# Kernel tuning notes

Measured on AMD Instinct MI355X. Metric: run time of the kernel, lower is better.

The kernel has to match this reference:

```python
import jax, jax.numpy as jnp
import numpy as np
import math

H = 2048
NH = 16
NKV = 4
HD = H // NH  # 128
N_REP = NH // NKV
EPS = 1e-6


def rms_norm(x, w, eps=1e-6):
    x32 = x.astype(jnp.float32)
    y = x32 * jax.lax.rsqrt(jnp.mean(x32 * x32, axis=-1, keepdims=True) + eps)
    return (y * w.astype(jnp.float32)).astype(x.dtype)


def mha(normed, key_in, val_in, q_w, k_w, v_w, o_w, bias):
    # normed: [b,s,H]; key_in/val_in: [b,n,H]; bias broadcastable to [b,nh,s,n]
    b, s, _ = normed.shape
    n = key_in.shape[1]
    q = (normed @ q_w).reshape(b, s, NH, HD).transpose(0, 2, 1, 3)      # [b,nh,s,d]
    k = (key_in @ k_w).reshape(b, n, NKV, HD).transpose(0, 2, 1, 3)     # [b,nkv,n,d]
    v = (val_in @ v_w).reshape(b, n, NKV, HD).transpose(0, 2, 1, 3)
    k = jnp.repeat(k, N_REP, axis=1)  # GQA expand -> [b,nh,n,d]
    v = jnp.repeat(v, N_REP, axis=1)
    scores = jnp.einsum('bhsd,bhnd->bhsn', q, k) / math.sqrt(HD) + bias
    probs = jax.nn.softmax(scores.astype(jnp.float32), axis=-1).astype(q.dtype)
    out = jnp.einsum('bhsn,bhnd->bhsd', probs, v)
    out = out.transpose(0, 2, 1, 3).reshape(b, s, NH * HD) @ o_w
    return out, probs


def setup_inputs() -> dict:
    key = jax.random.key(0)
    ks = jax.random.split(key, 20)
    B, S, ND, T = 2, 2048, 64, 2048
    w = lambda k, sh: (jax.random.normal(k, sh, dtype=jnp.float32) * 0.02)
    return {
        'hidden_states': jax.random.normal(ks[0], (B, S, H), dtype=jnp.float32),
        'doc_summary_key': jax.random.normal(ks[1], (B, ND, H), dtype=jnp.float32),
        'doc_summary_value': jax.random.normal(ks[2], (B, ND, H), dtype=jnp.float32),
        'doc_summary_mask': jnp.ones((B, ND), dtype=jnp.float32),
        'token_key': jax.random.normal(ks[3], (B, T, H), dtype=jnp.float32),
        'token_value': jax.random.normal(ks[4], (B, T, H), dtype=jnp.float32),
        'token_mask': jnp.ones((B, T), dtype=jnp.float32),
        'cn_w': jnp.ones((H,), dtype=jnp.float32),
        'cq_w': w(ks[5], (H, NH * HD)),
        'ck_w': w(ks[6], (H, NKV * HD)),
        'cv_w': w(ks[7], (H, NKV * HD)),
        'co_w': w(ks[8], (NH * HD, H)),
        'c_gate': jnp.array([-1.0], dtype=jnp.float32),
        'fn_w': jnp.ones((H,), dtype=jnp.float32),
        'fq_w': w(ks[9], (H, NH * HD)),
        'fk_w': w(ks[10], (H, NKV * HD)),
        'fv_w': w(ks[11], (H, NKV * HD)),
        'fo_w': w(ks[12], (NH * HD, H)),
        'f_gate': jnp.array([-1.0], dtype=jnp.float32),
        'doc_token_map': jax.random.randint(ks[13], (B, T), 0, ND, dtype=jnp.int64)
            if jax.config.jax_enable_x64 else jax.random.randint(ks[13], (B, T), 0, ND).astype(jnp.int32),
    }


def reference(hidden_states, doc_summary_key, doc_summary_value, doc_summary_mask,
              token_key, token_value, token_mask,
              cn_w, cq_w, ck_w, cv_w, co_w, c_gate,
              fn_w, fq_w, fk_w, fv_w, fo_w, f_gate,
              doc_token_map):
    # ---- coarse stage: cross-attention over document summaries ----
    normed = rms_norm(hidden_states, cn_w)
    coarse_bias = ((1.0 - doc_summary_mask) * -1e9)[:, None, None, :]  # [b,1,1,nd]
    attn_out, probs = mha(normed, doc_summary_key, doc_summary_value,
                          cq_w, ck_w, cv_w, co_w, coarse_bias)
    doc_scores = probs.mean(axis=(1, 2))  # [b,nd] avg over heads+query positions
    gate_c = jax.nn.sigmoid(c_gate).astype(attn_out.dtype)
    out = hidden_states + gate_c * attn_out

    # ---- fine stage: cross-attention over token KV with log-doc-score bias ----
    log_ds = jnp.log(doc_scores + EPS)
    doc_bias = jnp.take_along_axis(log_ds, doc_token_map, axis=1)  # [b,T]
    pad_bias = (1.0 - token_mask) * -1e9
    fine_bias = (doc_bias + pad_bias)[:, None, None, :]  # [b,1,1,T]
    normed_f = rms_norm(out, fn_w)
    attn_out_f, _ = mha(normed_f, token_key, token_value,
                        fq_w, fk_w, fv_w, fo_w, fine_bias)
    gate_f = jax.nn.sigmoid(f_gate).astype(attn_out_f.dtype)
    final = out + gate_f * attn_out_f
    return final
```

## Files before the change

kernel.cpp:

```cpp
#include <hip/hip_runtime.h>
#include <hip/hip_bf16.h>

typedef unsigned short u16;
typedef unsigned int u32;
typedef __attribute__((ext_vector_type(8))) short bf16x8;
typedef __attribute__((ext_vector_type(4))) float f32x4;

constexpr int NH = 16;
constexpr int H = 2048;
constexpr float SCALE = 0.08838834764831845f;
constexpr float L2E = 1.4426950408889634f;
constexpr float SCALE2 = SCALE * L2E;
constexpr float THR2 = 8.0f * L2E;

__device__ __forceinline__ u16 f2bf(float f) {
    u32 u = __float_as_uint(f);
    u32 r = u + 0x7fffu + ((u >> 16) & 1u);
    return (u16)(r >> 16);
}
__device__ __forceinline__ u32 pack2(float x, float y) {
    return (u32)f2bf(x) | ((u32)f2bf(y) << 16);
}
__device__ __forceinline__ u32 pack2_cvt(float x, float y) {
    __hip_bfloat162 h = __float22bfloat162_rn(float2{x, y});
    return *reinterpret_cast<u32*>(&h);
}

#define GLD_LDS16(gsrc, ldst)                                                  \
    __builtin_amdgcn_global_load_lds(                                          \
        (const __attribute__((address_space(1))) void*)(gsrc),                 \
        (__attribute__((address_space(3))) void*)(ldst), 16, 0, 0)

__global__ __launch_bounds__(256) void cvt_f32_bf16_2(const float* __restrict__ a,
                                                      u16* __restrict__ oa,
                                                      const float* __restrict__ b,
                                                      u16* __restrict__ ob, int n4) {
    int i = blockIdx.x * 256 + threadIdx.x;
    const float* in;
    u16* out;
    if (i < n4) { in = a; out = oa; }
    else if (i < 2 * n4) { i -= n4; in = b; out = ob; }
    else return;
    float4 v = reinterpret_cast<const float4*>(in)[i];
    uint2 o;
    o.x = pack2(v.x, v.y);
    o.y = pack2(v.z, v.w);
    reinterpret_cast<uint2*>(out)[i] = o;
}

__global__ __launch_bounds__(256) void cvt_f32_bf16(const float* __restrict__ in,
                                                    u16* __restrict__ out, int n4) {
    int i = blockIdx.x * 256 + threadIdx.x;
    if (i >= n4) return;
    float4 v = reinterpret_cast<const float4*>(in)[i];
    uint2 o;
    o.x = pack2(v.x, v.y);
    o.y = pack2(v.z, v.w);
    reinterpret_cast<uint2*>(out)[i] = o;
}

__global__ __launch_bounds__(256)
void transpose_cvt4(const float* __restrict__ i0, const float* __restrict__ i1,
                    const float* __restrict__ i2, const float* __restrict__ i3,
                    u16* __restrict__ o0, u16* __restrict__ o1,
                    u16* __restrict__ o2, u16* __restrict__ o3, int K, int N) {
    const float* in = (blockIdx.z == 0) ? i0 : (blockIdx.z == 1) ? i1
                    : (blockIdx.z == 2) ? i2 : i3;
    u16* out = (blockIdx.z == 0) ? o0 : (blockIdx.z == 1) ? o1
             : (blockIdx.z == 2) ? o2 : o3;
    __shared__ u16 tile[32][33];
    int bn = blockIdx.x * 32, bk = blockIdx.y * 32;
    int tx = threadIdx.x & 31, ty = threadIdx.x >> 5;
#pragma unroll
    for (int r = 0; r < 32; r += 8)
        tile[tx][r + ty] = f2bf(in[(size_t)(bk + r + ty) * N + bn + tx]);
    __syncthreads();
#pragma unroll
    for (int r = 0; r < 32; r += 8)
        out[(size_t)(bn + r + ty) * K + bk + tx] = tile[r + ty][tx];
}

__global__ __launch_bounds__(256) void rmsnorm_kernel(const float* __restrict__ x,
                                                      const float* __restrict__ w,
                                                      u16* __restrict__ y) {
    int r = blockIdx.x;
    const float4* xr = reinterpret_cast<const float4*>(x + (size_t)r * H);
    int t = threadIdx.x;
    float4 v0 = xr[t * 2], v1 = xr[t * 2 + 1];
    float ss = v0.x * v0.x + v0.y * v0.y + v0.z * v0.z + v0.w * v0.w
             + v1.x * v1.x + v1.y * v1.y + v1.z * v1.z + v1.w * v1.w;
#pragma unroll
    for (int d = 1; d < 64; d <<= 1) ss += __shfl_xor(ss, d);
    __shared__ float red[4];
    if ((t & 63) == 0) red[t >> 6] = ss;
    __syncthreads();
    float tot = red[0] + red[1] + red[2] + red[3];
    float rs = rsqrtf(tot * (1.0f / H) + 1e-6f);
    const float4* wr = reinterpret_cast<const float4*>(w);
    float4 w0 = wr[t * 2], w1 = wr[t * 2 + 1];
    uint4 o;
    o.x = pack2(v0.x * rs * w0.x, v0.y * rs * w0.y);
    o.y = pack2(v0.z * rs * w0.z, v0.w * rs * w0.w);
    o.z = pack2(v1.x * rs * w1.x, v1.y * rs * w1.y);
    o.w = pack2(v1.z * rs * w1.z, v1.w * rs * w1.w);
    reinterpret_cast<uint4*>(y + (size_t)r * H)[t] = o;
}

template <int MODE, int BN>
__device__ __forceinline__
void gemm_body(const u16* __restrict__ A, const u16* __restrict__ Bt,
               u16* __restrict__ Cb, float* __restrict__ Cf,
               const float* __restrict__ resid, const float* __restrict__ gate_p,
               int N, int K, int brow, int bcol) {
    constexpr int WN = BN / 32;
    constexpr int BWROWS = BN / 4;
    __shared__ u16 As[2][128 * 64];
    __shared__ u16 Bs[2][BN * 64];
    const int t = threadIdx.x;
    const int lane = t & 63, wid = t >> 6;
    const int wm = wid >> 1, wn = wid & 1;
    const int l15 = lane & 15, hi = lane >> 4;
    const int rsw = l15 & 7;

    f32x4 acc[4][WN] = {};
    const int srow = lane >> 3;
    const int sseg = ((lane & 7) ^ srow) * 8;
    const u16* aBase = A + (size_t)(brow + wid * 32 + srow) * K + sseg;
    const u16* bBase = Bt + (size_t)(bcol + wid * BWROWS + srow) * K + sseg;

#define GSTAGE(KT, BF)                                                          \
    do {                                                                        \
        _Pragma("unroll")                                                       \
        for (int u = 0; u < 4; ++u)                                             \
            GLD_LDS16(aBase + (size_t)(u * 8) * K + (KT),                       \
                      &As[BF][(wid * 32 + u * 8) * 64]);                        \
        _Pragma("unroll")                                                       \
        for (int u = 0; u < BWROWS / 8; ++u)                                    \
            GLD_LDS16(bBase + (size_t)(u * 8) * K + (KT),                       \
                      &Bs[BF][(wid * BWROWS + u * 8) * 64]);                    \
    } while (0)

    GSTAGE(0, 0);
    __syncthreads();
    int buf = 0;
    for (int kt = 0; kt < K; kt += 64) {
        if (kt + 64 < K) GSTAGE(kt + 64, buf ^ 1);
        bf16x8 af[4][2], bfr[WN][2];
#pragma unroll
        for (int i = 0; i < 4; ++i) {
            int row = wm * 64 + i * 16 + l15;
#pragma unroll
            for (int ko = 0; ko < 2; ++ko)
                af[i][ko] = *reinterpret_cast<const bf16x8*>(
                    &As[buf][row * 64 + (((ko * 4 + hi) ^ rsw) * 8)]);
        }
#pragma unroll
        for (int j = 0; j < WN; ++j) {
            int row = wn * (BN / 2) + j * 16 + l15;
#pragma unroll
            for (int ko = 0; ko < 2; ++ko)
                bfr[j][ko] = *reinterpret_cast<const bf16x8*>(
                    &Bs[buf][row * 64 + (((ko * 4 + hi) ^ rsw) * 8)]);
        }
#pragma unroll
        for (int ko = 0; ko < 2; ++ko)
#pragma unroll
            for (int i = 0; i < 4; ++i)
#pragma unroll
                for (int j = 0; j < WN; ++j)
                    acc[i][j] = __builtin_amdgcn_mfma_f32_16x16x32_bf16(
                        af[i][ko], bfr[j][ko], acc[i][j], 0, 0, 0);
        __syncthreads();
        buf ^= 1;
    }
#undef GSTAGE

    float g = 0.f;
    if (MODE == 1) g = 1.0f / (1.0f + expf(-gate_p[0]));
    const int r0 = hi * 4, c0 = l15;
#pragma unroll
    for (int i = 0; i < 4; ++i) {
#pragma unroll
        for (int j = 0; j < WN; ++j) {
            int col = bcol + wn * (BN / 2) + j * 16 + c0;
#pragma unroll
            for (int r = 0; r < 4; ++r) {
                int row = brow + wm * 64 + i * 16 + r0 + r;
                float v = acc[i][j][r];
                if (MODE == 0) Cb[(size_t)row * N + col] = f2bf(v);
                else Cf[(size_t)row * N + col] = resid[(size_t)row * N + col] + g * v;
            }
        }
    }
}

template <int MODE, int BN>
__global__ __launch_bounds__(256)
void gemm_tn(const u16* __restrict__ A, const u16* __restrict__ Bt,
             u16* __restrict__ Cb, float* __restrict__ Cf,
             const float* __restrict__ resid, const float* __restrict__ gate_p,
             int M, int N, int K) {
    int nbx = gridDim.x;
    int nwg = nbx * gridDim.y;
    int lin = blockIdx.y * nbx + blockIdx.x;
    if (!(nwg & 7)) { int q = nwg >> 3; lin = (lin & 7) * q + (lin >> 3); }
    gemm_body<MODE, BN>(A, Bt, Cb, Cf, resid, gate_p, N, K,
                        (lin / nbx) * 128, (lin % nbx) * BN);
}

template <int MODE, int BN>
__global__ __launch_bounds__(256)
void gemm_tn_z2(const u16* __restrict__ A0, const u16* __restrict__ B0, u16* __restrict__ C0,
                const u16* __restrict__ A1, const u16* __restrict__ B1, u16* __restrict__ C1,
                int N, int K) {
    const u16* A = blockIdx.z ? A1 : A0;
    const u16* B = blockIdx.z ? B1 : B0;
    u16* C = blockIdx.z ? C1 : C0;
    gemm_body<MODE, BN>(A, B, C, nullptr, nullptr, nullptr, N, K,
                        blockIdx.y * 128, blockIdx.x * BN);
}

__global__ __launch_bounds__(256)
void coarse_attn(const u16* __restrict__ q, const u16* __restrict__ kc,
                 const u16* __restrict__ vc, const float* __restrict__ mask,
                 float* __restrict__ doc_part, u16* __restrict__ attn_c) {
    constexpr int SC = 2048 / 64;
    int bid = blockIdx.x;
    int b = bid / (NH * SC);
    int rem = bid % (NH * SC);
    int h = rem / SC, sc = rem % SC;
    int kv = h >> 2;
    int t = threadIdx.x, lane = t & 63, wid = t >> 6;
    const int l15 = lane & 15, k0 = (lane >> 4) * 8;

    __shared__ u16 Kt[64 * 136];
    __shared__ u16 Vt[128 * 72];
    __shared__ u16 Pt[4][16 * 72];
    __shared__ float p_acc[64];

    {
        int n = t >> 2, s2 = t & 3;
        const u16* src = kc + (size_t)(b * 64 + n) * 512 + kv * 128;
#pragma unroll
        for (int u = 0; u < 4; ++u) {
            int sg = s2 + u * 4;
            *reinterpret_cast<uint4*>(&Kt[n * 136 + sg * 8]) =
                *reinterpret_cast<const uint4*>(src + sg * 8);
        }
    }
    {
        int n = t & 63, dblk = t >> 6;
        const u16* src = vc + (size_t)(b * 64 + n) * 512 + kv * 128 + dblk * 32;
#pragma unroll
        for (int u = 0; u < 4; ++u) {
            u16 tmp[8];
            *reinterpret_cast<uint4*>(tmp) = *reinterpret_cast<const uint4*>(src + u * 8);
#pragma unroll
            for (int e = 0; e < 8; ++e) Vt[(dblk * 32 + u * 8 + e) * 72 + n] = tmp[e];
        }
    }
    if (t < 64) p_acc[t] = 0.f;
    __syncthreads();

    int qrow = sc * 64 + wid * 16 + l15;
    const u16* qsrc = q + (size_t)(b * 2048 + qrow) * 2048 + h * 128;
    bf16x8 af[4];
#pragma unroll
    for (int kk = 0; kk < 4; ++kk)
        af[kk] = *reinterpret_cast<const bf16x8*>(qsrc + kk * 32 + k0);

    f32x4 sc4[4] = {};
#pragma unroll
    for (int kk = 0; kk < 4; ++kk)
#pragma unroll
        for (int j = 0; j < 4; ++j) {
            bf16x8 bfr = *reinterpret_cast<const bf16x8*>(&Kt[(j * 16 + l15) * 136 + kk * 32 + k0]);
            sc4[j] = __builtin_amdgcn_mfma_f32_16x16x32_bf16(af[kk], bfr, sc4[j], 0, 0, 0);
        }

    float s[4][4];
#pragma unroll
    for (int j = 0; j < 4; ++j) {
        float bia = (1.0f - mask[b * 64 + j * 16 + l15]) * (-1e9f * L2E);
#pragma unroll
        for (int r = 0; r < 4; ++r) s[j][r] = sc4[j][r] * SCALE2 + bia;
    }
    float m4[4], l4[4];
#pragma unroll
    for (int r = 0; r < 4; ++r) {
        float m = fmaxf(fmaxf(s[0][r], s[1][r]), fmaxf(s[2][r], s[3][r]));
#pragma unroll
        for (int d = 1; d < 16; d <<= 1) m = fmaxf(m, __shfl_xor(m, d));
        m4[r] = m;
    }
#pragma unroll
    for (int r = 0; r < 4; ++r) {
        float l = 0.f;
#pragma unroll
        for (int j = 0; j < 4; ++j) { s[j][r] = exp2f(s[j][r] - m4[r]); l += s[j][r]; }
#pragma unroll
        for (int d = 1; d < 16; d <<= 1) l += __shfl_xor(l, d);
        l4[r] = l;
    }
#pragma unroll
    for (int j = 0; j < 4; ++j) {
        float cs = 0.f;
#pragma unroll
        for (int r = 0; r < 4; ++r) {
            float pr = s[j][r] / l4[r];
            Pt[wid][((lane >> 4) * 4 + r) * 72 + j * 16 + l15] = f2bf(pr);
            cs += pr;
        }
        cs += __shfl_xor(cs, 16);
        cs += __shfl_xor(cs, 32);
        if (lane < 16) atomicAdd(&p_acc[j * 16 + lane], cs);
    }
    __syncthreads();

    f32x4 o4[8] = {};
#pragma unroll
    for (int kk2 = 0; kk2 < 2; ++kk2) {
        bf16x8 a2 = *reinterpret_cast<const bf16x8*>(&Pt[wid][l15 * 72 + kk2 * 32 + k0]);
#pragma unroll
        for (int j2 = 0; j2 < 8; ++j2) {
            bf16x8 b2 = *reinterpret_cast<const bf16x8*>(&Vt[(j2 * 16 + l15) * 72 + kk2 * 32 + k0]);
            o4[j2] = __builtin_amdgcn_mfma_f32_16x16x32_bf16(a2, b2, o4[j2], 0, 0, 0);
        }
    }
#pragma unroll
    for (int j2 = 0; j2 < 8; ++j2)
#pragma unroll
        for (int r = 0; r < 4; ++r) {
            int row = sc * 64 + wid * 16 + (lane >> 4) * 4 + r;
            attn_c[(size_t)(b * 2048 + row) * 2048 + h * 128 + j2 * 16 + l15] = f2bf(o4[j2][r]);
        }
    if (t < 64) atomicAdd(&doc_part[(blockIdx.x & 7) * 128 + b * 64 + t], p_acc[t]);
}

__global__ __launch_bounds__(256)
void bias_kernel(const float* __restrict__ doc_part, const int* __restrict__ map,
                 const float* __restrict__ tmask, float* __restrict__ bias) {
    __shared__ float lg[128];
    int t = threadIdx.x;
    if (t < 128) {
        float s = 0.f;
#pragma unroll
        for (int i = 0; i < 8; ++i) s += doc_part[i * 128 + t];
        lg[t] = logf(s / 32768.0f + 1e-6f);
    }
    __syncthreads();
    int i = blockIdx.x * 256 + t;
    if (i >= 2 * 2048) return;
    int b = i >> 11;
    bias[i] = (lg[b * 64 + map[i]] + (1.0f - tmask[i]) * -1e9f) * L2E;
}

__global__ __launch_bounds__(256, 2)
void flash_attn(const u16* __restrict__ q, const u16* __restrict__ kf,
                const u16* __restrict__ vT, const float* __restrict__ bias,
                u16* __restrict__ attn_f) {
    int bid = blockIdx.x;
    int b = bid >> 8;
    int rem = bid & 255;
    int h = rem >> 4, sc = rem & 15;
    int kv = h >> 2;
    int t = threadIdx.x, lane = t & 63, wid = t >> 6;
    const int l15 = lane & 15, hi = lane >> 4;
    const int k0 = hi * 8;
    const int rswp = l15 & 7;

    __shared__ u16 Kt[2][64 * 128];
    __shared__ u16 Vt[2][128 * 64];
    __shared__ u16 Pt[4][32 * 64];

    bf16x8 qf4[2][4];
#pragma unroll
    for (int f = 0; f < 2; ++f) {
        int qrow = sc * 128 + wid * 32 + f * 16 + l15;
        const u16* qsrc = q + (size_t)(b * 2048 + qrow) * 2048 + h * 128;
#pragma unroll
        for (int kk = 0; kk < 4; ++kk)
            qf4[f][kk] = *reinterpret_cast<const bf16x8*>(qsrc + kk * 32 + k0);
    }

    const int krl = lane >> 4, kslot = lane & 15;
    const int vrl = lane >> 3, vslot = lane & 7;
    const u16* kbase = kf + (size_t)(b * 2048) * 512 + kv * 128;
    const u16* vbase = vT + (size_t)(kv * 128) * 4096 + b * 2048;
    const float* bbase = bias + b * 2048;

#define STAGE_K(TT, BF)                                                            \
    do {                                                                           \
        _Pragma("unroll")                                                          \
        for (int u = 0; u < 4; ++u) {                                              \
            int row = wid * 16 + u * 4 + krl;                                      \
            const u16* src = kbase + (size_t)((TT) + row) * 512                    \
                             + ((kslot ^ (row & 7)) * 8);                          \
            GLD_LDS16(src, &Kt[BF][(wid * 16 + u * 4) * 128]);                     \
        }                                                                          \
    } while (0)
#define STAGE_V(TT, BF)                                                            \
    do {                                                                           \
        _Pragma("unroll")                                                          \
        for (int u = 0; u < 4; ++u) {                                              \
            int row = wid * 32 + u * 8 + vrl;                                      \
            const u16* src = vbase + (size_t)row * 4096 + (TT)                     \
                             + ((vslot ^ (row & 7)) * 8);                          \
            GLD_LDS16(src, &Vt[BF][(wid * 32 + u * 8) * 64]);                      \
        }                                                                          \
    } while (0)

    float mstate[2] = {-1e30f, -1e30f}, lstate[2] = {0.f, 0.f};
    f32x4 o4[2][8] = {};

    STAGE_K(0, 0);
    STAGE_V(0, 0);
    __syncthreads();
    int par = 0;

    for (int t0 = 0; t0 < 2048; t0 += 64) {
        int t1 = (t0 + 64) & 2047;
        STAGE_K(t1, par ^ 1);
        STAGE_V(t1, par ^ 1);

        f32x4 st0[4] = {}, st1[4] = {};
        __builtin_amdgcn_s_setprio(1);
#pragma unroll
        for (int kk = 0; kk < 4; ++kk)
#pragma unroll
            for (int kb = 0; kb < 4; ++kb) {
                int row = kb * 16 + l15;
                bf16x8 kfrag = *reinterpret_cast<const bf16x8*>(
                    &Kt[par][row * 128 + (((kk * 4 + hi) ^ (row & 7)) * 8)]);
                st0[kb] = __builtin_amdgcn_mfma_f32_16x16x32_bf16(kfrag, qf4[0][kk], st0[kb], 0, 0, 0);
                st1[kb] = __builtin_amdgcn_mfma_f32_16x16x32_bf16(kfrag, qf4[1][kk], st1[kb], 0, 0, 0);
            }
        __builtin_amdgcn_s_setprio(0);

        float p[2][4][4];
        float pmax[2] = {-1e30f, -1e30f};
#pragma unroll
        for (int kb = 0; kb < 4; ++kb) {
            float4 b4 = *reinterpret_cast<const float4*>(bbase + t0 + kb * 16 + hi * 4);
            float bb[4] = {b4.x, b4.y, b4.z, b4.w};
#pragma unroll
            for (int r = 0; r < 4; ++r) {
                float v0 = st0[kb][r] * SCALE2 + bb[r];
                float v1 = st1[kb][r] * SCALE2 + bb[r];
                p[0][kb][r] = v0;
                p[1][kb][r] = v1;
                pmax[0] = fmaxf(pmax[0], v0);
                pmax[1] = fmaxf(pmax[1], v1);
            }
        }
#pragma unroll
        for (int f = 0; f < 2; ++f) {
            pmax[f] = fmaxf(pmax[f], __shfl_xor(pmax[f], 16));
            pmax[f] = fmaxf(pmax[f], __shfl_xor(pmax[f], 32));
        }

        bool need = (pmax[0] > mstate[0] + THR2) || (pmax[1] > mstate[1] + THR2);
        if (__any(need)) {
#pragma unroll
            for (int f = 0; f < 2; ++f) {
                float mnew = fmaxf(mstate[f], pmax[f]);
                float sco = exp2f(mstate[f] - mnew);
                float sco_out[4];
#pragma unroll
                for (int r = 0; r < 4; ++r) sco_out[r] = __shfl(sco, hi * 4 + r);
#pragma unroll
                for (int j2 = 0; j2 < 8; ++j2)
#pragma unroll
                    for (int r = 0; r < 4; ++r) o4[f][j2][r] *= sco_out[r];
                lstate[f] *= sco;
                mstate[f] = mnew;
            }
        }

#pragma unroll
        for (int f = 0; f < 2; ++f) {
            float lt = 0.f;
#pragma unroll
            for (int kb = 0; kb < 4; ++kb)
#pragma unroll
                for (int r = 0; r < 4; ++r) {
                    p[f][kb][r] = exp2f(p[f][kb][r] - mstate[f]);
                    lt += p[f][kb][r];
                }
            lt += __shfl_xor(lt, 16);
            lt += __shfl_xor(lt, 32);
            lstate[f] += lt;
        }

#pragma unroll
        for (int f = 0; f < 2; ++f)
#pragma unroll
            for (int kb = 0; kb < 4; ++kb) {
                uint2 w;
                w.x = pack2_cvt(p[f][kb][0], p[f][kb][1]);
                w.y = pack2_cvt(p[f][kb][2], p[f][kb][3]);
                int idx = (f * 16 + l15) * 64
                        + (((kb * 2 + (hi >> 1)) ^ rswp) * 8) + (hi & 1) * 4;
                *reinterpret_cast<uint2*>(&Pt[wid][idx]) = w;
            }

        __builtin_amdgcn_s_setprio(1);
#pragma unroll
        for (int kc = 0; kc < 2; ++kc) {
            bf16x8 pa0 = *reinterpret_cast<const bf16x8*>(
                &Pt[wid][l15 * 64 + (((kc * 4 + hi) ^ rswp) * 8)]);
            bf16x8 pa1 = *reinterpret_cast<const bf16x8*>(
                &Pt[wid][(16 + l15) * 64 + (((kc * 4 + hi) ^ rswp) * 8)]);
#pragma unroll
            for (int j2 = 0; j2 < 8; ++j2) {
                int d = j2 * 16 + l15;
                bf16x8 vb = *reinterpret_cast<const bf16x8*>(
                    &Vt[par][d * 64 + (((kc * 4 + hi) ^ (d & 7)) * 8)]);
                o4[0][j2] = __builtin_amdgcn_mfma_f32_16x16x32_bf16(pa0, vb, o4[0][j2], 0, 0, 0);
                o4[1][j2] = __builtin_amdgcn_mfma_f32_16x16x32_bf16(pa1, vb, o4[1][j2], 0, 0, 0);
            }
        }
        __builtin_amdgcn_s_setprio(0);
        __syncthreads();
        par ^= 1;
    }
#undef STAGE_K
#undef STAGE_V

#pragma unroll
    for (int f = 0; f < 2; ++f) {
        float linv[4];
#pragma unroll
        for (int r = 0; r < 4; ++r) linv[r] = 1.0f / __shfl(lstate[f], hi * 4 + r);
#pragma unroll
        for (int j2 = 0; j2 < 8; ++j2)
#pragma unroll
            for (int r = 0; r < 4; ++r) {
                int row = sc * 128 + wid * 32 + f * 16 + hi * 4 + r;
                attn_f[(size_t)(b * 2048 + row) * 2048 + h * 128 + j2 * 16 + l15] =
                    f2bf(o4[f][j2][r] * linv[r]);
            }
    }
}

extern "C" void kernel_launch(void* const* d_in, const int* in_sizes, int n_in,
                              void* d_out, int out_size, void* d_ws, size_t ws_size,
                              hipStream_t stream) {
    const float* hidden = (const float*)d_in[0];
    const float* dsk    = (const float*)d_in[1];
    const float* dsv    = (const float*)d_in[2];
    const float* dsmask = (const float*)d_in[3];
    const float* tk     = (const float*)d_in[4];
    const float* tv     = (const float*)d_in[5];
    const float* tmask  = (const float*)d_in[6];
    const float* cn_w   = (const float*)d_in[7];
    const float* cq_w   = (const float*)d_in[8];
    const float* ck_w   = (const float*)d_in[9];
    const float* cv_w   = (const float*)d_in[10];
    const float* co_w   = (const float*)d_in[11];
    const float* c_gate = (const float*)d_in[12];
    const float* fn_w   = (const float*)d_in[13];
    const float* fq_w   = (const float*)d_in[14];
    const float* fk_w   = (const float*)d_in[15];
    const float* fv_w   = (const float*)d_in[16];
    const float* fo_w   = (const float*)d_in[17];
    const float* f_gate = (const float*)d_in[18];
    const int*   map    = (const int*)d_in[19];
    float* out_f = (float*)d_out;

    char* ws = (char*)d_ws;
    size_t off = 0;
    auto alloc = [&](size_t bytes) {
        char* p = ws + off;
        off += (bytes + 255) & ~(size_t)255;
        return p;
    };
    u16*  normA = (u16*)alloc(4096ULL * 2048 * 2);
    u16*  qbuf  = (u16*)alloc(4096ULL * 2048 * 2);
    u16*  kc    = (u16*)alloc(128ULL * 512 * 2);
    u16*  vc    = (u16*)alloc(128ULL * 512 * 2);
    u16*  dskb  = (u16*)alloc(128ULL * 2048 * 2);
    u16*  dsvb  = (u16*)alloc(128ULL * 2048 * 2);
    u16*  kfb   = (u16*)alloc(4096ULL * 512 * 2);
    u16*  vTb   = (u16*)alloc(512ULL * 4096 * 2);
    u16*  cqT   = (u16*)alloc(2048ULL * 2048 * 2);
    u16*  ckT   = (u16*)alloc(512ULL * 2048 * 2);
    u16*  cvT   = (u16*)alloc(512ULL * 2048 * 2);
    u16*  coT   = (u16*)alloc(2048ULL * 2048 * 2);
    u16*  fqT   = (u16*)alloc(2048ULL * 2048 * 2);
    u16*  fkT   = (u16*)alloc(512ULL * 2048 * 2);
    u16*  fvT   = (u16*)alloc(512ULL * 2048 * 2);
    u16*  foT   = (u16*)alloc(2048ULL * 2048 * 2);
    float* doc_part = (float*)alloc(8 * 128 * 4);
    float* biasb    = (float*)alloc(4096 * 4);

    hipMemsetAsync(doc_part, 0, 8 * 128 * 4, stream);

    transpose_cvt4<<<dim3(64, 64, 4), 256, 0, stream>>>(cq_w, co_w, fq_w, fo_w,
                                                        cqT, coT, fqT, foT, 2048, 2048);
    transpose_cvt4<<<dim3(16, 64, 4), 256, 0, stream>>>(ck_w, cv_w, fk_w, fv_w,
                                                        ckT, cvT, fkT, fvT, 2048, 512);

    cvt_f32_bf16_2<<<(2 * 128 * 2048 / 4 + 255) / 256, 256, 0, stream>>>(
        dsk, dskb, dsv, dsvb, 128 * 2048 / 4);
    rmsnorm_kernel<<<4096, 256, 0, stream>>>(hidden, cn_w, normA);

    gemm_tn<0, 128><<<dim3(16, 32), 256, 0, stream>>>(normA, cqT, qbuf, nullptr, nullptr, nullptr, 4096, 2048, 2048);
    gemm_tn_z2<0, 64><<<dim3(8, 1, 2), 256, 0, stream>>>(dskb, ckT, kc, dsvb, cvT, vc, 512, 2048);

    coarse_attn<<<1024, 256, 0, stream>>>(qbuf, kc, vc, dsmask, doc_part, normA);
    bias_kernel<<<16, 256, 0, stream>>>(doc_part, map, tmask, biasb);

    gemm_tn<1, 128><<<dim3(16, 32), 256, 0, stream>>>(normA, coT, nullptr, out_f, hidden, c_gate, 4096, 2048, 2048);

    rmsnorm_kernel<<<4096, 256, 0, stream>>>(out_f, fn_w, qbuf);
    gemm_tn<0, 128><<<dim3(16, 32), 256, 0, stream>>>(qbuf, fqT, normA, nullptr, nullptr, nullptr, 4096, 2048, 2048);
    cvt_f32_bf16<<<(4096 * 2048 / 4 + 255) / 256, 256, 0, stream>>>(tk, qbuf, 4096 * 2048 / 4);
    gemm_tn<0, 64><<<dim3(8, 32), 256, 0, stream>>>(qbuf, fkT, kfb, nullptr, nullptr, nullptr, 4096, 512, 2048);
    cvt_f32_bf16<<<(4096 * 2048 / 4 + 255) / 256, 256, 0, stream>>>(tv, qbuf, 4096 * 2048 / 4);
    gemm_tn<0, 64><<<dim3(64, 4), 256, 0, stream>>>(fvT, qbuf, vTb, nullptr, nullptr, nullptr, 512, 4096, 2048);

    flash_attn<<<512, 256, 0, stream>>>(normA, kfb, vTb, biasb, qbuf);

    gemm_tn<1, 128><<<dim3(16, 32), 256, 0, stream>>>(qbuf, foT, nullptr, out_f, out_f, f_gate, 4096, 2048, 2048);
}
```

Baseline: 448.9 us.

## Split fine attention KV into halves with merge kernel; shrink GEMM tiles

Fine-stage flash attention now splits the 2048-token KV range into two halves across twice as many blocks. Each block uses smaller 32-token tiles and less LDS, and launch bounds allow 4 blocks per CU. A new merge kernel combines the unnormalized bf16 partial outputs using the saved (max, sum) stats. Two coarse-stage GEMMs switch to 64-wide tiles to launch more blocks. This is meant to raise occupancy and fill the GPU with 512 blocks previously, at the cost of extra partial-output traffic, an extra launch, and bf16 rounding of the partials.

```diff
diff --git a/kernel.cpp b/kernel.cpp
--- a/kernel.cpp
+++ b/kernel.cpp
@@ -24,6 +24,10 @@
 __device__ __forceinline__ u32 pack2_cvt(float x, float y) {
     __hip_bfloat162 h = __float22bfloat162_rn(float2{x, y});
     return *reinterpret_cast<u32*>(&h);
+}
+__device__ __forceinline__ float bf2f(u16 v) {
+    u32 u = (u32)v << 16;
+    return __uint_as_float(u);
 }
 
 #define GLD_LDS16(gsrc, ldst)                                                  \
@@ -355,23 +359,22 @@
     bias[i] = (lg[b * 64 + map[i]] + (1.0f - tmask[i]) * -1e9f) * L2E;
 }
 
-__global__ __launch_bounds__(256, 2)
+__global__ __launch_bounds__(256, 4)
 void flash_attn(const u16* __restrict__ q, const u16* __restrict__ kf,
                 const u16* __restrict__ vT, const float* __restrict__ bias,
-                u16* __restrict__ attn_f) {
+                u16* __restrict__ Opart, float2* __restrict__ Ml) {
     int bid = blockIdx.x;
-    int b = bid >> 8;
-    int rem = bid & 255;
-    int h = rem >> 4, sc = rem & 15;
+    int half = bid >> 9;
+    int rem = bid & 511;
+    int b = rem >> 8, h = (rem >> 4) & 15, sc = rem & 15;
     int kv = h >> 2;
     int t = threadIdx.x, lane = t & 63, wid = t >> 6;
     const int l15 = lane & 15, hi = lane >> 4;
     const int k0 = hi * 8;
-    const int rswp = l15 & 7;
-
-    __shared__ u16 Kt[2][64 * 128];
-    __shared__ u16 Vt[2][128 * 64];
-    __shared__ u16 Pt[4][32 * 64];
+
+    __shared__ u16 Kt[2][32 * 128];
+    __shared__ u16 Vt[2][128 * 32];
+    __shared__ u16 Pt[4][32 * 32];
 
     bf16x8 qf4[2][4];
 #pragma unroll
@@ -384,29 +387,29 @@
     }
 
     const int krl = lane >> 4, kslot = lane & 15;
-    const int vrl = lane >> 3, vslot = lane & 7;
-    const u16* kbase = kf + (size_t)(b * 2048) * 512 + kv * 128;
-    const u16* vbase = vT + (size_t)(kv * 128) * 4096 + b * 2048;
-    const float* bbase = bias + b * 2048;
+    const int vrl = lane >> 2, vslot = lane & 3;
+    const u16* kbase = kf + (size_t)(b * 2048) * 512 + kv * 128 + (size_t)(half * 1024) * 512;
+    const u16* vbase = vT + (size_t)(kv * 128) * 4096 + b * 2048 + half * 1024;
+    const float* bbase = bias + b * 2048 + half * 1024;
 
 #define STAGE_K(TT, BF)                                                            \
     do {                                                                           \
         _Pragma("unroll")                                                          \
-        for (int u = 0; u < 4; ++u) {                                              \
-            int row = wid * 16 + u * 4 + krl;                                      \
+        for (int u = 0; u < 2; ++u) {                                              \
+            int row = wid * 8 + u * 4 + krl;                                       \
             const u16* src = kbase + (size_t)((TT) + row) * 512                    \
                              + ((kslot ^ (row & 7)) * 8);                          \
-            GLD_LDS16(src, &Kt[BF][(wid * 16 + u * 4) * 128]);                     \
+            GLD_LDS16(src, &Kt[BF][(wid * 8 + u * 4) * 128]);                      \
         }                                                                          \
     } while (0)
 #define STAGE_V(TT, BF)                                                            \
     do {                                                                           \
         _Pragma("unroll")                                                          \
-        for (int u = 0; u < 4; ++u) {                                              \
-            int row = wid * 32 + u * 8 + vrl;                                      \
+        for (int u = 0; u < 2; ++u) {                                              \
+            int row = wid * 32 + u * 16 + vrl;                                     \
             const u16* src = vbase + (size_t)row * 4096 + (TT)                     \
-                             + ((vslot ^ (row & 7)) * 8);                          \
-            GLD_LDS16(src, &Vt[BF][(wid * 32 + u * 8) * 64]);                      \
+                             + ((vslot ^ (row & 3)) * 8);                          \
+            GLD_LDS16(src, &Vt[BF][(wid * 32 + u * 16) * 32]);                     \
         }                                                                          \
     } while (0)
 
@@ -418,17 +421,17 @@
     __syncthreads();
     int par = 0;
 
-    for (int t0 = 0; t0 < 2048; t0 += 64) {
-        int t1 = (t0 + 64) & 2047;
+    for (int t0 = 0; t0 < 1024; t0 += 32) {
+        int t1 = (t0 + 32) & 1023;
         STAGE_K(t1, par ^ 1);
         STAGE_V(t1, par ^ 1);
 
-        f32x4 st0[4] = {}, st1[4] = {};
+        f32x4 st0[2] = {}, st1[2] = {};
         __builtin_amdgcn_s_setprio(1);
 #pragma unroll
         for (int kk = 0; kk < 4; ++kk)
 #pragma unroll
-            for (int kb = 0; kb < 4; ++kb) {
+            for (int kb = 0; kb < 2; ++kb) {
                 int row = kb * 16 + l15;
                 bf16x8 kfrag = *reinterpret_cast<const bf16x8*>(
                     &Kt[par][row * 128 + (((kk * 4 + hi) ^ (row & 7)) * 8)]);
@@ -437,10 +440,10 @@
             }
         __builtin_amdgcn_s_setprio(0);
 
-        float p[2][4][4];
+        float p[2][2][4];
         float pmax[2] = {-1e30f, -1e30f};
 #pragma unroll
-        for (int kb = 0; kb < 4; ++kb) {
+        for (int kb = 0; kb < 2; ++kb) {
             float4 b4 = *reinterpret_cast<const float4*>(bbase + t0 + kb * 16 + hi * 4);
             float bb[4] = {b4.x, b4.y, b4.z, b4.w};
 #pragma unroll
@@ -481,7 +484,7 @@
         for (int f = 0; f < 2; ++f) {
             float lt = 0.f;
 #pragma unroll
-            for (int kb = 0; kb < 4; ++kb)
+            for (int kb = 0; kb < 2; ++kb)
 #pragma unroll
                 for (int r = 0; r < 4; ++r) {
                     p[f][kb][r] = exp2f(p[f][kb][r] - mstate[f]);
@@ -495,30 +498,27 @@
 #pragma unroll
         for (int f = 0; f < 2; ++f)
 #pragma unroll
-            for (int kb = 0; kb < 4; ++kb) {
+            for (int kb = 0; kb < 2; ++kb) {
                 uint2 w;
                 w.x = pack2_cvt(p[f][kb][0], p[f][kb][1]);
                 w.y = pack2_cvt(p[f][kb][2], p[f][kb][3]);
-                int idx = (f * 16 + l15) * 64
-                        + (((kb * 2 + (hi >> 1)) ^ rswp) * 8) + (hi & 1) * 4;
+                int idx = (f * 16 + l15) * 32
+                        + (((kb * 2 + (hi >> 1)) ^ (l15 & 3)) * 8) + (hi & 1) * 4;
                 *reinterpret_cast<uint2*>(&Pt[wid][idx]) = w;
             }
 
         __builtin_amdgcn_s_setprio(1);
-#pragma unroll
-        for (int kc = 0; kc < 2; ++kc) {
-            bf16x8 pa0 = *reinterpret_cast<const bf16x8*>(
-                &Pt[wid][l15 * 64 + (((kc * 4 + hi) ^ rswp) * 8)]);
-            bf16x8 pa1 = *reinterpret_cast<const bf16x8*>(
-                &Pt[wid][(16 + l15) * 64 + (((kc * 4 + hi) ^ rswp) * 8)]);
-#pragma unroll
-            for (int j2 = 0; j2 < 8; ++j2) {
-                int d = j2 * 16 + l15;
-                bf16x8 vb = *reinterpret_cast<const bf16x8*>(
-                    &Vt[par][d * 64 + (((kc * 4 + hi) ^ (d & 7)) * 8)]);
-                o4[0][j2] = __builtin_amdgcn_mfma_f32_16x16x32_bf16(pa0, vb, o4[0][j2], 0, 0, 0);
-                o4[1][j2] = __builtin_amdgcn_mfma_f32_16x16x32_bf16(pa1, vb, o4[1][j2], 0, 0, 0);
-            }
+        bf16x8 pa0 = *reinterpret_cast<const bf16x8*>(
+            &Pt[wid][l15 * 32 + ((hi ^ (l15 & 3)) * 8)]);
+        bf16x8 pa1 = *reinterpret_cast<const bf16x8*>(
+            &Pt[wid][(16 + l15) * 32 + ((hi ^ (l15 & 3)) * 8)]);
+#pragma unroll
+        for (int j2 = 0; j2 < 8; ++j2) {
+            int d = j2 * 16 + l15;
+            bf16x8 vb = *reinterpret_cast<const bf16x8*>(
+                &Vt[par][d * 32 + ((hi ^ (d & 3)) * 8)]);
+            o4[0][j2] = __builtin_amdgcn_mfma_f32_16x16x32_bf16(pa0, vb, o4[0][j2], 0, 0, 0);
+            o4[1][j2] = __builtin_amdgcn_mfma_f32_16x16x32_bf16(pa1, vb, o4[1][j2], 0, 0, 0);
         }
         __builtin_amdgcn_s_setprio(0);
         __syncthreads();
@@ -527,20 +527,44 @@
 #undef STAGE_K
 #undef STAGE_V
 
+    size_t pbase = ((size_t)(half * 512 + rem) * 128) * 128;
 #pragma unroll
     for (int f = 0; f < 2; ++f) {
-        float linv[4];
-#pragma unroll
-        for (int r = 0; r < 4; ++r) linv[r] = 1.0f / __shfl(lstate[f], hi * 4 + r);
 #pragma unroll
         for (int j2 = 0; j2 < 8; ++j2)
 #pragma unroll
             for (int r = 0; r < 4; ++r) {
-                int row = sc * 128 + wid * 32 + f * 16 + hi * 4 + r;
-                attn_f[(size_t)(b * 2048 + row) * 2048 + h * 128 + j2 * 16 + l15] =
-                    f2bf(o4[f][j2][r] * linv[r]);
+                int lrow = wid * 32 + f * 16 + hi * 4 + r;
+                Opart[pbase + (size_t)lrow * 128 + j2 * 16 + l15] = f2bf(o4[f][j2][r]);
             }
-    }
+        if (hi == 0)
+            Ml[(size_t)(half * 512 + rem) * 128 + wid * 32 + f * 16 + l15] =
+                make_float2(mstate[f], lstate[f]);
+    }
+}
+
+__global__ __launch_bounds__(256)
+void merge_attn(const u16* __restrict__ Opart, const float2* __restrict__ Ml,
+                u16* __restrict__ attn_f) {
+    int flat = blockIdx.x * 256 + threadIdx.x;
+    int row = flat >> 4;
+    int d0 = (flat & 15) * 8;
+    int p = row >> 7, qi = row & 127;
+    int b = p >> 8, h = (p >> 4) & 15, sc = p & 15;
+    float2 ml1 = Ml[row];
+    float2 ml2 = Ml[65536 + row];
+    float m = fmaxf(ml1.x, ml2.x);
+    float s1 = exp2f(ml1.x - m), s2 = exp2f(ml2.x - m);
+    float linv = 1.0f / (ml1.y * s1 + ml2.y * s2);
+    s1 *= linv; s2 *= linv;
+    bf16x8 o1 = *reinterpret_cast<const bf16x8*>(&Opart[(size_t)row * 128 + d0]);
+    bf16x8 o2 = *reinterpret_cast<const bf16x8*>(&Opart[(size_t)(65536 + row) * 128 + d0]);
+    u16 out[8];
+#pragma unroll
+    for (int e = 0; e < 8; ++e)
+        out[e] = f2bf(bf2f((u16)o1[e]) * s1 + bf2f((u16)o2[e]) * s2);
+    size_t off = ((size_t)(b * 2048 + sc * 128 + qi)) * 2048 + h * 128 + d0;
+    *reinterpret_cast<uint4*>(&attn_f[off]) = *reinterpret_cast<uint4*>(out);
 }
 
 extern "C" void kernel_launch(void* const* d_in, const int* in_sizes, int n_in,
@@ -591,6 +615,8 @@
     u16*  fkT   = (u16*)alloc(512ULL * 2048 * 2);
     u16*  fvT   = (u16*)alloc(512ULL * 2048 * 2);
     u16*  foT   = (u16*)alloc(2048ULL * 2048 * 2);
+    u16*  OpartB = (u16*)alloc(2ULL * 65536 * 128 * 2);
+    float* MlB   = (float*)alloc(2ULL * 65536 * 8);
     float* doc_part = (float*)alloc(8 * 128 * 4);
     float* biasb    = (float*)alloc(4096 * 4);
 
@@ -605,13 +631,13 @@
         dsk, dskb, dsv, dsvb, 128 * 2048 / 4);
     rmsnorm_kernel<<<4096, 256, 0, stream>>>(hidden, cn_w, normA);
 
-    gemm_tn<0, 128><<<dim3(16, 32), 256, 0, stream>>>(normA, cqT, qbuf, nullptr, nullptr, nullptr, 4096, 2048, 2048);
+    gemm_tn<0, 64><<<dim3(32, 32), 256, 0, stream>>>(normA, cqT, qbuf, nullptr, nullptr, nullptr, 4096, 2048, 2048);
     gemm_tn_z2<0, 64><<<dim3(8, 1, 2), 256, 0, stream>>>(dskb, ckT, kc, dsvb, cvT, vc, 512, 2048);
 
     coarse_attn<<<1024, 256, 0, stream>>>(qbuf, kc, vc, dsmask, doc_part, normA);
     bias_kernel<<<16, 256, 0, stream>>>(doc_part, map, tmask, biasb);
 
-    gemm_tn<1, 128><<<dim3(16, 32), 256, 0, stream>>>(normA, coT, nullptr, out_f, hidden, c_gate, 4096, 2048, 2048);
+    gemm_tn<1, 64><<<dim3(32, 32), 256, 0, stream>>>(normA, coT, nullptr, out_f, hidden, c_gate, 4096, 2048, 2048);
 
     rmsnorm_kernel<<<4096, 256, 0, stream>>>(out_f, fn_w, qbuf);
     gemm_tn<0, 128><<<dim3(16, 32), 256, 0, stream>>>(qbuf, fqT, normA, nullptr, nullptr, nullptr, 4096, 2048, 2048);
@@ -620,7 +646,8 @@
     cvt_f32_bf16<<<(4096 * 2048 / 4 + 255) / 256, 256, 0, stream>>>(tv, qbuf, 4096 * 2048 / 4);
     gemm_tn<0, 64><<<dim3(64, 4), 256, 0, stream>>>(fvT, qbuf, vTb, nullptr, nullptr, nullptr, 512, 4096, 2048);
 
-    flash_attn<<<512, 256, 0, stream>>>(normA, kfb, vTb, biasb, qbuf);
+    flash_attn<<<1024, 256, 0, stream>>>(normA, kfb, vTb, biasb, OpartB, (float2*)MlB);
+    merge_attn<<<4096, 256, 0, stream>>>(OpartB, (const float2*)MlB, qbuf);
 
     gemm_tn<1, 128><<<dim3(16, 32), 256, 0, stream>>>(qbuf, foT, nullptr, out_f, out_f, f_gate, 4096, 2048, 2048);
 }
```

Result: slower. 633.9 us (+41.2%).
